# Performance work log

Measured on AMD Instinct MI355X. Metric: run time of the kernel, lower is better.

## Reference

```python
import jax, jax.numpy as jnp
import numpy as np
import math

BS = 32; N_NODE = 400; N = BS * N_NODE; E = 204800
D = 200; HS = 1024; SEQ = 512
N_NTYPE = 4; N_ETYPE = 38
HEADS = 4; DPH = D // HEADS
K_LAYERS = 5
EP1 = 1.0


def _lin(key, fi, fo, lead=None):
    shape = (fi, fo) if lead is None else (lead, fi, fo)
    return jax.random.normal(key, shape, jnp.float32) * 0.05


def setup_inputs() -> dict:
    key = jax.random.key(0)
    ks = jax.random.split(key, 20)
    inp = {}
    inp['hidden_states'] = jax.random.normal(ks[0], (BS, SEQ, HS), jnp.float32)
    inp['X'] = jax.random.normal(ks[1], (N, D), jnp.float32)
    inp['node_feature_extra'] = jax.random.normal(ks[2], (N, D), jnp.float32)
    inp['edge_index'] = jax.random.randint(ks[3], (2, E), 0, N)
    inp['edge_type'] = jax.random.randint(ks[4], (E,), 0, N_ETYPE)
    inp['node_type'] = jax.random.randint(ks[5], (N,), 0, N_NTYPE)
    inp['epoch'] = 0
    edge_in = N_ETYPE + 1 + 2 * N_NTYPE  # one-hot edge type (+self-loop) + head/tail node-type one-hots
    inp['We1'] = _lin(ks[6], edge_in, D); inp['be1'] = jnp.zeros((D,), jnp.float32)
    inp['We2'] = _lin(ks[7], D, D);       inp['be2'] = jnp.zeros((D,), jnp.float32)
    inp['Wkey'] = _lin(ks[8], 3 * D, D, K_LAYERS);  inp['bkey'] = jnp.zeros((K_LAYERS, D), jnp.float32)
    inp['Wmsg'] = _lin(ks[9], 3 * D, D, K_LAYERS);  inp['bmsg'] = jnp.zeros((K_LAYERS, D), jnp.float32)
    inp['Wqry'] = _lin(ks[10], 2 * D, D, K_LAYERS); inp['bqry'] = jnp.zeros((K_LAYERS, D), jnp.float32)
    inp['Wm1'] = _lin(ks[11], D, D, K_LAYERS);      inp['bm1'] = jnp.zeros((K_LAYERS, D), jnp.float32)
    inp['Wm2'] = _lin(ks[12], D, D, K_LAYERS);      inp['bm2'] = jnp.zeros((K_LAYERS, D), jnp.float32)
    inp['Wq_att'] = _lin(ks[13], D, D); inp['bq_att'] = jnp.zeros((D,), jnp.float32)
    inp['Wk_att'] = _lin(ks[14], D, D); inp['bk_att'] = jnp.zeros((D,), jnp.float32)
    inp['Wv_att'] = _lin(ks[15], D, D); inp['bv_att'] = jnp.zeros((D,), jnp.float32)
    inp['Wproj'] = _lin(ks[16], HS, D); inp['bproj'] = jnp.zeros((D,), jnp.float32)
    return inp


def _segment_softmax(scores, seg, n):
    m = jax.ops.segment_max(scores, seg, num_segments=n)
    m = jnp.where(jnp.isfinite(m), m, 0.0)
    e = jnp.exp(scores - m[seg])
    s = jax.ops.segment_sum(e, seg, num_segments=n)
    return e / (s[seg] + 1e-16)


def _gat_layer(X, nfe, src, dst, edge_emb, Wk, bk, Wm, bm, Wq, bq, W1, b1, W2, b2):
    n = X.shape[0]
    x = jnp.concatenate([X, nfe], axis=1)            # [N, 2D]
    x_i = x[dst]; x_j = x[src]                       # [E', 2D]
    key = (jnp.concatenate([x_i, edge_emb], 1) @ Wk + bk).reshape(-1, HEADS, DPH)
    msg = (jnp.concatenate([x_j, edge_emb], 1) @ Wm + bm).reshape(-1, HEADS, DPH)
    qry = ((x_i @ Wq + bq).reshape(-1, HEADS, DPH)) / math.sqrt(DPH)
    scores = (qry * key).sum(-1)                     # [E', HEADS]
    alpha = _segment_softmax(scores, src, n)
    cnt = jax.ops.segment_sum(jnp.ones_like(alpha[:, 0]), src, num_segments=n)[src]
    alpha = alpha * cnt[:, None]                     # scale by src out-degree (QAGNN GATConvE)
    out_msg = (msg * alpha[..., None]).reshape(-1, D)
    aggr = jax.ops.segment_sum(out_msg, dst, num_segments=n)
    out = jax.nn.relu(aggr @ W1 + b1) @ W2 + b2      # MLP, BatchNorm(eval) ~ identity
    sensitivity = jnp.max(jnp.linalg.norm(out, axis=-1))
    return out, sensitivity


def _forward(hidden_states, X, node_feature_extra, edge_index, edge_type, node_type,
             We1, be1, We2, be2, Wkey, bkey, Wmsg, bmsg, Wqry, bqry, Wm1, bm1, Wm2, bm2,
             Wq_att, bq_att, Wk_att, bk_att, Wv_att, bv_att, Wproj, bproj):
    n = X.shape[0]
    # self loops with edge type n_etype, as in GATConvE
    loop = jnp.arange(n)
    src = jnp.concatenate([edge_index[0], loop])
    dst = jnp.concatenate([edge_index[1], loop])
    et = jnp.concatenate([edge_type, jnp.full((n,), N_ETYPE, edge_type.dtype)])
    edge_vec = jax.nn.one_hot(et, N_ETYPE + 1, dtype=X.dtype)
    hvec = jax.nn.one_hot(node_type[src], N_NTYPE, dtype=X.dtype)
    tvec = jax.nn.one_hot(node_type[dst], N_NTYPE, dtype=X.dtype)
    # shared edge encoder (same edges each layer -> hoisted, identical math)
    edge_emb = jax.nn.relu(jnp.concatenate([edge_vec, hvec, tvec], 1) @ We1 + be1) @ We2 + be2
    context = hidden_states[:, 0, :] @ Wproj + bproj  # [bs, D]
    K = (context @ Wk_att + bk_att)[:, None, :]       # [bs, 1, D]
    V = (context @ Wv_att + bv_att)[:, None, :]
    nkey = jax.random.key(123)
    _X = X
    for li in range(K_LAYERS):
        _X, sens = _gat_layer(_X, node_feature_extra, src, dst, edge_emb,
                              Wkey[li], bkey[li], Wmsg[li], bmsg[li], Wqry[li], bqry[li],
                              Wm1[li], bm1[li], Wm2[li], bm2[li])
        _X = jax.nn.gelu(_X, approximate=False)
        Xb = _X.reshape(BS, N_NODE, D)
        Q = Xb @ Wq_att + bq_att
        Q = Q / jnp.maximum(jnp.linalg.norm(Q, axis=-1, keepdims=True), 1e-12)
        att = jnp.einsum('bnd,bmd->bnm', Q, K) / math.sqrt(D)  # [bs, n_node, 1]
        scale = jax.lax.stop_gradient(sens / (EP1 / 4.0))      # Laplace DP noise (non-diff in orig)
        noise = scale * jax.random.laplace(jax.random.fold_in(nkey, li), att.shape, att.dtype)
        att = att + noise
        _X = jnp.einsum('bnm,bmd->bnd', att, V).reshape(-1, D)
    return _X


def reference(hidden_states, X, node_feature_extra, edge_index, edge_type, node_type, epoch,
              We1, be1, We2, be2, Wkey, bkey, Wmsg, bmsg, Wqry, bqry, Wm1, bm1, Wm2, bm2,
              Wq_att, bq_att, Wk_att, bk_att, Wv_att, bv_att, Wproj, bproj):
    return _forward(hidden_states, X, node_feature_extra, edge_index, edge_type, node_type,
                    We1, be1, We2, be2, Wkey, bkey, Wmsg, bmsg, Wqry, bqry, Wm1, bm1, Wm2, bm2,
                    Wq_att, bq_att, Wk_att, bk_att, Wv_att, bv_att, Wproj, bproj)
```

## Files before the change

kernel.cpp:

```cpp
#include <hip/hip_runtime.h>
#include <stdint.h>

#define NBATCH 32
#define NNODE  400
#define NN     12800
#define NE     204800
#define EPE    217600
#define DD     200
#define NETYPE 38
#define NCOMBO 624
#define HSZ    1024
#define SEQQ   512
#define NL     5

__device__ __forceinline__ unsigned short f2bf(float x){
  uint32_t u = __float_as_uint(x);
  uint32_t r = (u + 0x7fffu + ((u>>16)&1u)) >> 16;
  return (unsigned short)r;
}

__device__ __forceinline__ uint32_t rotl32(uint32_t x, uint32_t d){ return (x<<d)|(x>>(32u-d)); }

__device__ void tf2x32(uint32_t k0, uint32_t k1, uint32_t x0, uint32_t x1,
                       uint32_t* o0, uint32_t* o1){
  uint32_t ks0=k0, ks1=k1, ks2=k0^k1^0x1BD11BDAu;
  uint32_t ks[3]={ks0,ks1,ks2};
  x0 += ks0; x1 += ks1;
  const uint32_t rotA[4]={13,15,26,6};
  const uint32_t rotB[4]={17,29,16,24};
  #pragma unroll
  for (int i=0;i<5;i++){
    const uint32_t* r = (i&1)? rotB : rotA;
    #pragma unroll
    for (int j=0;j<4;j++){ x0 += x1; x1 = rotl32(x1, r[j]); x1 ^= x0; }
    x0 += ks[(i+1)%3];
    x1 += ks[(i+2)%3] + (uint32_t)(i+1);
  }
  *o0=x0; *o1=x1;
}

__global__ void k_noise(float* noise){
  int i = blockIdx.x*256+threadIdx.x;
  if (i >= NL*NN) return;
  int l = i / NN, j = i % NN;
  uint32_t k0,k1,o0,o1,bits;
  tf2x32(0u,123u,0u,(uint32_t)l,&k0,&k1);
  tf2x32(k0,k1,0u,(uint32_t)j,&o0,&o1);
  bits = o0 ^ o1;
  uint32_t fb = (bits>>9) | 0x3f800000u;
  float f = __uint_as_float(fb) - 1.0f;
  const float minv = -0.99999994039535522461f;
  float u = fmaxf(minv, f*2.0f + minv);
  float s = (u>0.f)?1.f:((u<0.f)?-1.f:0.f);
  noise[i] = s*log1pf(-fabsf(u));
}

__global__ void k_edges(const int* eidx, int* outdeg, int* indeg){
  int e = blockIdx.x*256+threadIdx.x; if (e>=EPE) return;
  int s,dv;
  if (e < NE){ s = eidx[e]; dv = eidx[NE+e]; } else { s = dv = e-NE; }
  atomicAdd(&outdeg[s],1); atomicAdd(&indeg[dv],1);
}

__global__ void k_scan(const int* outdeg, const int* indeg, int* sstart, int* dstart){
  __shared__ int buf[2][1024];
  for (int which=0; which<2; ++which){
    const int* a = which? indeg : outdeg;
    int* o = which? dstart : sstart;
    int t = threadIdx.x;
    int c0 = t*13;
    int s = 0;
    for (int i=c0;i<c0+13;i++) if (i<NN) s += a[i];
    __syncthreads();
    buf[0][t]=s; __syncthreads();
    int cur=0;
    #pragma unroll
    for (int off=1; off<1024; off<<=1){
      int v = buf[cur][t];
      if (t>=off) v += buf[cur][t-off];
      buf[cur^1][t]=v; cur^=1; __syncthreads();
    }
    int run = buf[cur][t] - s;
    for (int i=c0;i<c0+13;i++) if (i<NN){ o[i]=run; run+=a[i]; }
    if (t==0) o[NN]=EPE;
  }
}

__global__ void k_scatter(const int* eidx, const int* etype, const int* ntype,
                          const int* sstart, const int* dstart, int* sfill, int* dfill,
                          int* s_dst, int* s_combo, int* d_src, int* d_combo, int* d_spos){
  int e = blockIdx.x*256+threadIdx.x; if (e>=EPE) return;
  int s,dv,et;
  if (e<NE){ s=eidx[e]; dv=eidx[NE+e]; et=etype[e]; } else { s=dv=e-NE; et=NETYPE; }
  int c = et*16 + ntype[s]*4 + ntype[dv];
  int p = sstart[s] + atomicAdd(&sfill[s],1);
  s_dst[p]=dv; s_combo[p]=c;
  int q = dstart[dv] + atomicAdd(&dfill[dv],1);
  d_src[q]=s; d_combo[q]=c; d_spos[q]=p;
}

__global__ void k_ehid(const float* We1, const float* be1, float* ehid){
  int i = blockIdx.x*256+threadIdx.x; if (i>=NCOMBO*DD) return;
  int c = i/DD, d = i%DD;
  int et=c>>4, ht=(c>>2)&3, tt=c&3;
  float v = We1[et*DD+d] + We1[(39+ht)*DD+d] + We1[(43+tt)*DD+d] + be1[d];
  ehid[i] = fmaxf(v,0.f);
}

__global__ void k_cvt_xcat(const float* X, const float* nfe, unsigned short* xbf){
  int i=blockIdx.x*256+threadIdx.x; if (i>=NN*448) return;
  int n=i/448, d=i%448;
  float v = (d<200)? X[(size_t)n*200+d] : (d<400)? nfe[(size_t)n*200+(d-200)] : 0.f;
  xbf[i] = f2bf(v);
}
__global__ void k_cvt_nfe(const float* nfe, unsigned short* nbf){
  int i=blockIdx.x*256+threadIdx.x; if (i>=NN*224) return;
  int n=i/224, d=i%224;
  nbf[i] = (d<200)? f2bf(nfe[(size_t)n*200+d]) : 0;
}

struct WJob { const float* src; unsigned short* dst; int Ksrc; int Kpad; };
struct WArgs { WJob j[26]; };
__global__ void k_wswz(WArgs a){
  WJob jb = a.j[blockIdx.z];
  int i = blockIdx.x*256+threadIdx.x;
  if (i >= jb.Kpad*256) return;
  int k = i>>8, n = i&255;
  unsigned short v = 0;
  if (k<jb.Ksrc && n<200) v = f2bf(jb.src[(size_t)k*200+n]);
  jb.dst[(((size_t)(k>>3))*256 + n)*8 + (k&7)] = v;
}

typedef __attribute__((ext_vector_type(8))) short bf16x8;
typedef __attribute__((ext_vector_type(4))) float f32x4;

struct MJob { const unsigned short* A; const unsigned short* B; const float* bias;
              float* C; unsigned short* Cbf; const float* r1v; const float* r1m;
              int relu; float scale; int gelu; };
struct MArgs { int Kpad; MJob j[3]; };

__global__ __launch_bounds__(256) void k_mgemm(MArgs g){
  const MJob jb = g.j[blockIdx.z];
  const int lane = threadIdx.x&63, w = threadIdx.x>>6;
  const int lr = lane&15, lk = lane>>4;
  const int m0 = blockIdx.y*128 + w*32;
  const int n0 = blockIdx.x*64;
  const int Kp = g.Kpad;
  f32x4 acc[2][4] = {};
  const unsigned short* a0 = jb.A + (size_t)(m0+lr)*Kp + lk*8;
  const unsigned short* a1 = a0 + (size_t)16*Kp;
  for (int ks=0; ks<Kp; ks+=32){
    bf16x8 af0 = *(const bf16x8*)(a0 + ks);
    bf16x8 af1 = *(const bf16x8*)(a1 + ks);
    const unsigned short* bb = jb.B + (((size_t)(ks>>3) + lk)*256 + n0 + lr)*8;
    bf16x8 b0 = *(const bf16x8*)(bb);
    bf16x8 b1 = *(const bf16x8*)(bb + 128);
    bf16x8 b2 = *(const bf16x8*)(bb + 256);
    bf16x8 b3 = *(const bf16x8*)(bb + 384);
    acc[0][0]=__builtin_amdgcn_mfma_f32_16x16x32_bf16(af0,b0,acc[0][0],0,0,0);
    acc[0][1]=__builtin_amdgcn_mfma_f32_16x16x32_bf16(af0,b1,acc[0][1],0,0,0);
    acc[0][2]=__builtin_amdgcn_mfma_f32_16x16x32_bf16(af0,b2,acc[0][2],0,0,0);
    acc[0][3]=__builtin_amdgcn_mfma_f32_16x16x32_bf16(af0,b3,acc[0][3],0,0,0);
    acc[1][0]=__builtin_amdgcn_mfma_f32_16x16x32_bf16(af1,b0,acc[1][0],0,0,0);
    acc[1][1]=__builtin_amdgcn_mfma_f32_16x16x32_bf16(af1,b1,acc[1][1],0,0,0);
    acc[1][2]=__builtin_amdgcn_mfma_f32_16x16x32_bf16(af1,b2,acc[1][2],0,0,0);
    acc[1][3]=__builtin_amdgcn_mfma_f32_16x16x32_bf16(af1,b3,acc[1][3],0,0,0);
  }
  #pragma unroll
  for (int mt=0; mt<2; ++mt){
    int mbase = m0 + mt*16 + lk*4;
    #pragma unroll
    for (int nt=0; nt<4; ++nt){
      int n = n0 + nt*16 + lr;
      #pragma unroll
      for (int r=0;r<4;r++){
        int m = mbase + r;
        float v = acc[mt][nt][r];
        if (n < 200){
          if (jb.r1v)  v += jb.r1v[m]*jb.r1m[(size_t)(m/NNODE)*200 + n];
          if (jb.bias) v += jb.bias[n];
          v *= jb.scale;
          if (jb.relu) v = fmaxf(v, 0.f);
          if (jb.C)    jb.C[(size_t)m*200 + n] = v;
          if (jb.Cbf){
            float o = jb.gelu? 0.5f*v*(1.0f+erff(v*0.70710678118654752440f)) : v;
            jb.Cbf[(size_t)m*224 + n] = f2bf(o);
          }
        } else if (jb.Cbf && n < 224){
          jb.Cbf[(size_t)m*224 + n] = 0;
        }
      }
    }
  }
}

struct RJob { const float* A; const float* W; const float* bias; float* C; int K; size_t lda; };
struct RArgs { RJob j[12]; float* part; int NS; int Kc; };
__global__ __launch_bounds__(256) void k_rowpart(RArgs a){
  RJob jb = a.j[blockIdx.z];
  int m = blockIdx.x, s = blockIdx.y;
  int k0 = s*a.Kc, k1 = k0 + a.Kc; if (k1 > jb.K) k1 = jb.K;
  int kc = k1 - k0;
  __shared__ float row[128];
  const float* ap = jb.A + (size_t)m*jb.lda + k0;
  for (int k=threadIdx.x; k<kc; k+=256) row[k]=ap[k];
  __syncthreads();
  int n = threadIdx.x;
  if (n < 200){
    float acc = 0.f;
    const float* wp = jb.W + (size_t)k0*200 + n;
    for (int kk=0; kk<kc; ++kk) acc += row[kk]*wp[(size_t)kk*200];
    a.part[(((size_t)blockIdx.z*32 + m)*8 + s)*200 + n] = acc;
  }
}
__global__ __launch_bounds__(256) void k_rowred(RArgs a){
  RJob jb = a.j[blockIdx.z];
  int m = blockIdx.x, n = threadIdx.x;
  if (n >= 200) return;
  float acc = jb.bias? jb.bias[n] : 0.f;
  for (int s=0; s<a.NS; ++s) acc += a.part[(((size_t)blockIdx.z*32 + m)*8 + s)*200 + n];
  jb.C[(size_t)m*200+n] = acc;
}

struct Job {
  const float* A; const float* W; const float* bias; float* C;
  const float* r1v; const float* r1m; int relu;
};
struct GArgs { int M,N,K,lda; Job j[12]; };

#define BMT 64
#define BNT 64
#define BKT 16

__global__ __launch_bounds__(256) void k_gemm(GArgs g){
  const Job jb = g.j[blockIdx.z];
  const int m0 = blockIdx.y*BMT, n0 = blockIdx.x*BNT;
  __shared__ float As[BKT][BMT+4];
  __shared__ float Bs[BKT][BNT+4];
  float acc[4][4]={};
  const int t = threadIdx.x;
  const int tx = t & 15, ty = t >> 4;
  for (int k0=0; k0<g.K; k0+=BKT){
    {
      int r = t>>2, cq = t&3;
      int m = m0+r, k = k0+cq*4;
      float4 v = make_float4(0.f,0.f,0.f,0.f);
      if (m < g.M && k < g.K){
        if (k+3 < g.K) v = *(const float4*)(jb.A + (size_t)m*g.lda + k);
        else {
          const float* ap = jb.A + (size_t)m*g.lda;
          float tm[4]={0.f,0.f,0.f,0.f};
          for (int qq=0;qq<4;qq++) if (k+qq<g.K) tm[qq]=ap[k+qq];
          v = make_float4(tm[0],tm[1],tm[2],tm[3]);
        }
      }
      As[cq*4+0][r]=v.x; As[cq*4+1][r]=v.y; As[cq*4+2][r]=v.z; As[cq*4+3][r]=v.w;
    }
    {
      int r = t>>4, cq = t&15;
      int k = k0+r, n = n0+cq*4;
      float4 v = make_float4(0.f,0.f,0.f,0.f);
      if (k < g.K && n < g.N){
        if (n+3 < g.N) v = *(const float4*)(jb.W + (size_t)k*g.N + n);
        else { const float* wp = jb.W + (size_t)k*g.N;
          float tm[4]={0.f,0.f,0.f,0.f};
          for (int qq=0;qq<4;qq++) if (n+qq<g.N) tm[qq]=wp[n+qq];
          v = make_float4(tm[0],tm[1],tm[2],tm[3]); }
      }
      Bs[r][cq*4+0]=v.x; Bs[r][cq*4+1]=v.y; Bs[r][cq*4+2]=v.z; Bs[r][cq*4+3]=v.w;
    }
    __syncthreads();
    int kend = g.K-k0; if (kend>BKT) kend=BKT;
    for (int kk=0;kk<kend;kk++){
      float4 av = *(const float4*)&As[kk][ty*4];
      float4 bv = *(const float4*)&Bs[kk][tx*4];
      float a[4]={av.x,av.y,av.z,av.w};
      float b[4]={bv.x,bv.y,bv.z,bv.w};
      #pragma unroll
      for (int i=0;i<4;i++){
        #pragma unroll
        for (int jq=0;jq<4;jq++) acc[i][jq] += a[i]*b[jq];
      }
    }
    __syncthreads();
  }
  #pragma unroll
  for (int i=0;i<4;i++){
    int m = m0+ty*4+i; if (m>=g.M) continue;
    int bidx = m / NNODE;
    #pragma unroll
    for (int jq=0;jq<4;jq++){
      int n = n0+tx*4+jq; if (n>=g.N) continue;
      float v = acc[i][jq];
      if (jb.bias) v += jb.bias[n];
      if (jb.r1v)  v += jb.r1v[m]*jb.r1m[(size_t)bidx*g.N + n];
      if (jb.relu) v = fmaxf(v,0.f);
      jb.C[(size_t)m*g.N+n] = v;
    }
  }
}

__global__ void k_prep(const float* qv, const float* Ak, float* ps){
  int wid = threadIdx.x>>6, lane = threadIdx.x&63;
  int n = blockIdx.x*4 + wid; if (n>=NN) return;
  float acch[4]={0.f,0.f,0.f,0.f};
  for (int d=lane; d<DD; d+=64)
    acch[d/50] += qv[(size_t)n*DD+d]*Ak[(size_t)n*DD+d];
  for (int off=1; off<64; off<<=1){
    #pragma unroll
    for (int h=0;h<4;h++) acch[h] += __shfl_xor(acch[h], off);
  }
  if (lane==0){
    #pragma unroll
    for (int h=0;h<4;h++) ps[n*4+h]=acch[h];
  }
}

__global__ __launch_bounds__(256) void k_score(const int* s_dst, const int* s_combo, const float* qv,
                        const float* Bk, const float* ps, float* scores){
  int p = blockIdx.x*64 + (threadIdx.x>>2);
  if (p>=EPE) return;
  int sub = threadIdx.x&3;
  int dv = s_dst[p], c = s_combo[p];
  const float4* qr = (const float4*)(qv + (size_t)dv*DD);
  const float4* br = (const float4*)(Bk + (size_t)c*DD);
  float acc[4]={0.f,0.f,0.f,0.f};
  #pragma unroll
  for (int i=0;i<13;i++){
    int q = sub + 4*i;
    if (q < 50){
      float4 a = qr[q], b = br[q];
      int d = q*4;
      acc[(d+0)/50] += a.x*b.x;
      acc[(d+1)/50] += a.y*b.y;
      acc[(d+2)/50] += a.z*b.z;
      acc[(d+3)/50] += a.w*b.w;
    }
  }
  #pragma unroll
  for (int off=1; off<4; off<<=1){
    #pragma unroll
    for (int h=0;h<4;h++) acc[h] += __shfl_xor(acc[h], off);
  }
  scores[(size_t)p*4+sub] = ps[dv*4+sub] + acc[sub];
}

__global__ void k_softmax(const int* sstart, float* scores){
  int n = blockIdx.x;
  int st = sstart[n], en = sstart[n+1];
  int cnt = en-st;
  int t = threadIdx.x;
  float mx = -3.402823466e38f;
  for (int i=t; i<cnt*4; i+=64) mx = fmaxf(mx, scores[(size_t)(st+(i>>2))*4 + (i&3)]);
  for (int off=4; off<64; off<<=1) mx = fmaxf(mx, __shfl_xor(mx,off));
  float sm=0.f;
  for (int i=t; i<cnt*4; i+=64) sm += expf(scores[(size_t)(st+(i>>2))*4 + (i&3)] - mx);
  for (int off=4; off<64; off<<=1) sm += __shfl_xor(sm,off);
  float scale = (float)cnt / (sm + 1e-16f);
  for (int i=t; i<cnt*4; i+=64){
    size_t idx=(size_t)(st+(i>>2))*4+(i&3);
    scores[idx] = expf(scores[idx]-mx)*scale;
  }
}

__global__ void k_aggr(const int* dstart, const int* d_src, const int* d_combo, const int* d_spos,
                       const float* alpha, const float* Am, const float* Bm,
                       unsigned short* aggr_bf){
  int v = blockIdx.x; int d = threadIdx.x; if (d>=224) return;
  if (d>=200){ aggr_bf[(size_t)v*224+d]=0; return; }
  int h = d/50;
  int st=dstart[v], en=dstart[v+1];
  float acc=0.f;
  for (int q=st;q<en;q++){
    int s=d_src[q], c=d_combo[q], p=d_spos[q];
    float a = alpha[(size_t)p*4+h];
    acc += a*(Am[(size_t)s*DD+d] + Bm[(size_t)c*DD+d]);
  }
  aggr_bf[(size_t)v*224+d]=f2bf(acc);
}

__global__ void k_sens(const float* out, float* sens2, int l){
  __shared__ float smax[4];
  int wid = threadIdx.x>>6, lane = threadIdx.x&63;
  int gw = blockIdx.x*4 + wid;
  float mx = 0.f;
  for (int n = gw; n < NN; n += 256){
    const float4* row = (const float4*)(out + (size_t)n*DD);
    float ss = 0.f;
    if (lane < 50){ float4 v = row[lane]; ss = v.x*v.x + v.y*v.y + v.z*v.z + v.w*v.w; }
    for (int off=1; off<64; off<<=1) ss += __shfl_xor(ss, off);
    mx = fmaxf(mx, ss);
  }
  if (lane==0) smax[wid] = mx;
  __syncthreads();
  if (threadIdx.x==0){
    float m = fmaxf(fmaxf(smax[0],smax[1]),fmaxf(smax[2],smax[3]));
    atomicMax((int*)&sens2[l], __float_as_int(m));
  }
}

__global__ void k_att(const float* Q, const float* Katt, const float* Vatt,
                      const float* sens2, const float* noise, int l,
                      float* att, float* outX){
  int wid=threadIdx.x>>6, lane=threadIdx.x&63;
  int n=blockIdx.x*4+wid; if (n>=NN) return;
  int b=n/NNODE;
  float qq=0.f, qk=0.f;
  for (int d=lane; d<DD; d+=64){
    float q=Q[(size_t)n*DD+d];
    qq += q*q; qk += q*Katt[b*DD+d];
  }
  for (int off=1;off<64;off<<=1){ qq+=__shfl_xor(qq,off); qk+=__shfl_xor(qk,off); }
  float nrm = fmaxf(sqrtf(qq), 1e-12f);
  float a = (qk/nrm) * 0.07071067811865475244f;
  a += 4.0f*sqrtf(sens2[l]) * noise[(size_t)l*NN + n];
  if (lane==0) att[n]=a;
  if (outX){
    for (int d=lane; d<DD; d+=64) outX[(size_t)n*DD+d] = a*Vatt[b*DD+d];
  }
}

static inline Job mkjob(const float* A, const float* W, const float* bias, float* C,
                        const float* r1v, const float* r1m, int relu){
  Job j; j.A=A; j.W=W; j.bias=bias; j.C=C; j.r1v=r1v; j.r1m=r1m; j.relu=relu; return j;
}

static inline void gemm_launch(hipStream_t stream, int M,int N,int K,int lda,
                               const Job* jobs, int nj){
  GArgs g; g.M=M; g.N=N; g.K=K; g.lda=lda;
  for (int i=0;i<nj;i++) g.j[i]=jobs[i];
  for (int i=nj;i<12;i++) g.j[i]=jobs[0];
  dim3 grid((N+BNT-1)/BNT,(M+BMT-1)/BMT,nj);
  k_gemm<<<grid,256,0,stream>>>(g);
}

static inline RJob mkrjob(const float* A, const float* W, const float* bias, float* C,
                          int K, size_t lda){
  RJob j; j.A=A; j.W=W; j.bias=bias; j.C=C; j.K=K; j.lda=lda; return j;
}

static inline void rgemm_launch(hipStream_t stream, const RJob* jobs, int nj,
                                float* part, int NS, int Kc){
  RArgs a;
  for (int i=0;i<nj;i++) a.j[i]=jobs[i];
  for (int i=nj;i<12;i++) a.j[i]=jobs[0];
  a.part = part; a.NS = NS; a.Kc = Kc;
  k_rowpart<<<dim3(NBATCH,NS,nj),256,0,stream>>>(a);
  k_rowred <<<dim3(NBATCH,1,nj),256,0,stream>>>(a);
}

static inline MJob mkmjob(const unsigned short* A, const unsigned short* B, const float* bias,
                          float* C, unsigned short* Cbf, const float* r1v, const float* r1m,
                          int relu, float scale, int gelu){
  MJob j; j.A=A; j.B=B; j.bias=bias; j.C=C; j.Cbf=Cbf; j.r1v=r1v; j.r1m=r1m;
  j.relu=relu; j.scale=scale; j.gelu=gelu; return j;
}

static inline void mgemm_launch(hipStream_t stream, int Kpad, const MJob* jobs, int nj){
  MArgs a; a.Kpad=Kpad;
  for (int i=0;i<nj;i++) a.j[i]=jobs[i];
  for (int i=nj;i<3;i++) a.j[i]=jobs[0];
  k_mgemm<<<dim3(4,100,nj),256,0,stream>>>(a);
}

extern "C" void kernel_launch(void* const* d_in, const int* in_sizes, int n_in,
                              void* d_out, int out_size, void* d_ws, size_t ws_size,
                              hipStream_t stream){
  const float* hs    = (const float*)d_in[0];
  const float* X     = (const float*)d_in[1];
  const float* nfe   = (const float*)d_in[2];
  const int*   eidx  = (const int*)d_in[3];
  const int*   etype = (const int*)d_in[4];
  const int*   ntype = (const int*)d_in[5];
  const float* We1   = (const float*)d_in[7];
  const float* be1   = (const float*)d_in[8];
  const float* We2   = (const float*)d_in[9];
  const float* be2   = (const float*)d_in[10];
  const float* Wkey  = (const float*)d_in[11];
  const float* bkey  = (const float*)d_in[12];
  const float* Wmsg  = (const float*)d_in[13];
  const float* bmsg  = (const float*)d_in[14];
  const float* Wqry  = (const float*)d_in[15];
  const float* bqry  = (const float*)d_in[16];
  const float* Wm1   = (const float*)d_in[17];
  const float* bm1   = (const float*)d_in[18];
  const float* Wm2   = (const float*)d_in[19];
  const float* bm2   = (const float*)d_in[20];
  const float* Wq_att= (const float*)d_in[21];
  const float* bq_att= (const float*)d_in[22];
  const float* Wk_att= (const float*)d_in[23];
  const float* bk_att= (const float*)d_in[24];
  const float* Wv_att= (const float*)d_in[25];
  const float* bv_att= (const float*)d_in[26];
  const float* Wproj = (const float*)d_in[27];
  const float* bproj = (const float*)d_in[28];
  float* outp = (float*)d_out;

  char* cur = (char*)d_ws;
  auto allocf = [&](size_t n)->float*{ float* p=(float*)cur; cur += ((n*4+255)/256)*256; return p; };
  auto alloci = [&](size_t n)->int*  { int*   p=(int*)cur;   cur += ((n*4+255)/256)*256; return p; };
  auto allocb = [&](size_t n)->unsigned short*{ unsigned short* p=(unsigned short*)cur; cur += ((n*2+255)/256)*256; return p; };

  float* noise  = allocf((size_t)NL*NN);
  float* ehid   = allocf((size_t)NCOMBO*DD);
  float* eemb   = allocf((size_t)NCOMBO*DD);
  float* Bk     = allocf((size_t)NL*NCOMBO*DD);
  float* Bm     = allocf((size_t)NL*NCOMBO*DD);
  float* context= allocf((size_t)NBATCH*DD);
  float* Katt   = allocf((size_t)NBATCH*DD);
  float* Vatt   = allocf((size_t)NBATCH*DD);
  float* CKk    = allocf((size_t)4*NBATCH*DD);
  float* CKm    = allocf((size_t)4*NBATCH*DD);
  float* CKq    = allocf((size_t)4*NBATCH*DD);
  float* Ak     = allocf((size_t)NN*DD);
  float* Am     = allocf((size_t)NN*DD);
  float* Aq     = allocf((size_t)NN*DD);
  float* ps     = allocf((size_t)NN*4);
  float* scores = allocf((size_t)EPE*4);
  float* Q      = allocf((size_t)NN*DD);
  float* outb   = allocf((size_t)NN*DD);
  float* att    = allocf((size_t)NN);
  float* sens2  = allocf(8);
  float* rpart  = allocf((size_t)12*NBATCH*8*200);
  unsigned short* xcat_bf = allocb((size_t)NN*448);
  unsigned short* nfe_bf  = allocb((size_t)NN*224);
  unsigned short* aggr_bf = allocb((size_t)NN*224);
  unsigned short* tmp1_bf = allocb((size_t)NN*224);
  unsigned short* gelu_bf = allocb((size_t)NN*224);
  unsigned short* wkx0  = allocb((size_t)448*256);
  unsigned short* wmx0  = allocb((size_t)448*256);
  unsigned short* wqx0  = allocb((size_t)448*256);
  unsigned short* wkN   = allocb((size_t)4*224*256);
  unsigned short* wmN   = allocb((size_t)4*224*256);
  unsigned short* wqN   = allocb((size_t)4*224*256);
  unsigned short* wm1s  = allocb((size_t)5*224*256);
  unsigned short* wm2s  = allocb((size_t)5*224*256);
  unsigned short* wqatts= allocb((size_t)224*256);
  int* sstart = alloci(NN+1);
  int* dstart = alloci(NN+1);
  int* outdeg = alloci(NN);
  int* indeg  = alloci(NN);
  int* sfill  = alloci(NN);
  int* dfill  = alloci(NN);
  int* s_dst  = alloci(EPE);
  int* s_combo= alloci(EPE);
  int* d_src  = alloci(EPE);
  int* d_combo= alloci(EPE);
  int* d_spos = alloci(EPE);
  if ((size_t)(cur-(char*)d_ws) > ws_size) return;

  hipMemsetAsync(outdeg,0,(size_t)4*NN*4,stream);
  hipMemsetAsync(sens2 ,0,32,stream);

  k_noise<<<(NL*NN+255)/256,256,0,stream>>>(noise);
  k_edges<<<(EPE+255)/256,256,0,stream>>>(eidx,outdeg,indeg);
  k_scan<<<1,1024,0,stream>>>(outdeg,indeg,sstart,dstart);
  k_scatter<<<(EPE+255)/256,256,0,stream>>>(eidx,etype,ntype,sstart,dstart,sfill,dfill,
                                            s_dst,s_combo,d_src,d_combo,d_spos);
  k_ehid<<<(NCOMBO*DD+255)/256,256,0,stream>>>(We1,be1,ehid);
  { Job j = mkjob(ehid,We2,be2,eemb,0,0,0); gemm_launch(stream,NCOMBO,DD,DD,DD,&j,1); }
  { Job js[10];
    for (int l=0;l<NL;l++){
      js[2*l+0]=mkjob(eemb, Wkey + (size_t)l*600*DD + 400*DD, 0, Bk + (size_t)l*NCOMBO*DD, 0,0,0);
      js[2*l+1]=mkjob(eemb, Wmsg + (size_t)l*600*DD + 400*DD, bmsg + (size_t)l*DD,
                      Bm + (size_t)l*NCOMBO*DD, 0,0,0);
    }
    gemm_launch(stream,NCOMBO,DD,DD,DD,js,10);
  }
  k_cvt_xcat<<<(NN*448+255)/256,256,0,stream>>>(X,nfe,xcat_bf);
  k_cvt_nfe<<<(NN*224+255)/256,256,0,stream>>>(nfe,nfe_bf);
  { WArgs wa; int wn=0;
    auto addw=[&](const float* s, unsigned short* d, int Ks, int Kp){
      wa.j[wn].src=s; wa.j[wn].dst=d; wa.j[wn].Ksrc=Ks; wa.j[wn].Kpad=Kp; wn++; };
    addw(Wkey, wkx0, 400,448);
    addw(Wmsg, wmx0, 400,448);
    addw(Wqry, wqx0, 400,448);
    for (int l=1;l<NL;l++){
      addw(Wkey + (size_t)l*600*DD + 200*DD, wkN + (size_t)(l-1)*224*256, 200,224);
      addw(Wmsg + (size_t)l*600*DD + 200*DD, wmN + (size_t)(l-1)*224*256, 200,224);
      addw(Wqry + (size_t)l*400*DD + 200*DD, wqN + (size_t)(l-1)*224*256, 200,224);
    }
    for (int l=0;l<NL;l++){
      addw(Wm1 + (size_t)l*DD*DD, wm1s + (size_t)l*224*256, 200,224);
      addw(Wm2 + (size_t)l*DD*DD, wm2s + (size_t)l*224*256, 200,224);
    }
    addw(Wq_att, wqatts, 200,224);
    k_wswz<<<dim3(448,1,wn),256,0,stream>>>(wa);
  }
  { RJob j = mkrjob(hs, Wproj, bproj, context, HSZ, (size_t)SEQQ*HSZ);
    rgemm_launch(stream, &j, 1, rpart, 8, 128); }
  { RJob js[2] = { mkrjob(context, Wk_att, bk_att, Katt, DD, DD),
                   mkrjob(context, Wv_att, bv_att, Vatt, DD, DD) };
    rgemm_launch(stream, js, 2, rpart, 2, 100); }
  { RJob js[12];
    for (int l=1;l<NL;l++){
      js[3*(l-1)+0]=mkrjob(Vatt, Wkey + (size_t)l*600*DD, 0, CKk + (size_t)(l-1)*NBATCH*DD, DD, DD);
      js[3*(l-1)+1]=mkrjob(Vatt, Wmsg + (size_t)l*600*DD, 0, CKm + (size_t)(l-1)*NBATCH*DD, DD, DD);
      js[3*(l-1)+2]=mkrjob(Vatt, Wqry + (size_t)l*400*DD, 0, CKq + (size_t)(l-1)*NBATCH*DD, DD, DD);
    }
    rgemm_launch(stream, js, 12, rpart, 4, 50);
  }

  const float invs = 0.14142135623730950488f;
  for (int l=0;l<NL;l++){
    const float* bkey_l = bkey + (size_t)l*DD;
    const float* bqry_l = bqry + (size_t)l*DD;
    const float* Bk_l = Bk + (size_t)l*NCOMBO*DD;
    const float* Bm_l = Bm + (size_t)l*NCOMBO*DD;

    if (l==0){
      MJob js[3] = { mkmjob(xcat_bf, wkx0, bkey_l, Ak, 0, 0,0,0, 1.f,0),
                     mkmjob(xcat_bf, wmx0, 0,      Am, 0, 0,0,0, 1.f,0),
                     mkmjob(xcat_bf, wqx0, bqry_l, Aq, 0, 0,0,0, invs,0) };
      mgemm_launch(stream,448,js,3);
    } else {
      const float* ckk = CKk + (size_t)(l-1)*NBATCH*DD;
      const float* ckm = CKm + (size_t)(l-1)*NBATCH*DD;
      const float* ckq = CKq + (size_t)(l-1)*NBATCH*DD;
      MJob js[3] = { mkmjob(nfe_bf, wkN + (size_t)(l-1)*224*256, bkey_l, Ak, 0, att, ckk, 0, 1.f,0),
                     mkmjob(nfe_bf, wmN + (size_t)(l-1)*224*256, 0,      Am, 0, att, ckm, 0, 1.f,0),
                     mkmjob(nfe_bf, wqN + (size_t)(l-1)*224*256, bqry_l, Aq, 0, att, ckq, 0, invs,0) };
      mgemm_launch(stream,224,js,3);
    }
    k_prep<<<NN/4,256,0,stream>>>(Aq,Ak,ps);
    k_score<<<(EPE*4+255)/256,256,0,stream>>>(s_dst,s_combo,Aq,Bk_l,ps,scores);
    k_softmax<<<NN,64,0,stream>>>(sstart,scores);
    k_aggr<<<NN,256,0,stream>>>(dstart,d_src,d_combo,d_spos,scores,Am,Bm_l,aggr_bf);
    { MJob j = mkmjob(aggr_bf, wm1s + (size_t)l*224*256, bm1 + (size_t)l*DD, 0, tmp1_bf, 0,0,1, 1.f,0);
      mgemm_launch(stream,224,&j,1); }
    { MJob j = mkmjob(tmp1_bf, wm2s + (size_t)l*224*256, bm2 + (size_t)l*DD, outb, gelu_bf, 0,0,0, 1.f,1);
      mgemm_launch(stream,224,&j,1); }
    k_sens<<<64,256,0,stream>>>(outb,sens2,l);
    { MJob j = mkmjob(gelu_bf, wqatts, bq_att, Q, 0, 0,0,0, 1.f,0);
      mgemm_launch(stream,224,&j,1); }
    k_att<<<NN/4,256,0,stream>>>(Q,Katt,Vatt,sens2,noise,l,att,(l==NL-1)? outp : (float*)0);
  }
}
```

Measured before the change: 1.248 ms.

## Store message tensors in bf16 and vectorize edge aggregation across waves

The message-projection GEMM now writes its output Am directly as bf16 with row stride 200, and Bm is converted once to bf16. The aggregation kernel is rewritten so each wave processes every fourth incoming edge, with 25 lanes each loading 8 bf16 values and a float4 of attention weights, followed by a shared-memory reduction across the four waves. This halves gather bytes and widens loads in the edge-gather loop, at the cost of extra bf16 rounding in the messages and an added conversion kernel.

```diff
diff --git a/kernel.cpp b/kernel.cpp
--- a/kernel.cpp
+++ b/kernel.cpp
@@ -17,6 +17,9 @@
   uint32_t u = __float_as_uint(x);
   uint32_t r = (u + 0x7fffu + ((u>>16)&1u)) >> 16;
   return (unsigned short)r;
+}
+__device__ __forceinline__ float bf2f(unsigned short b){
+  return __uint_as_float(((uint32_t)b)<<16);
 }
 
 __device__ __forceinline__ uint32_t rotl32(uint32_t x, uint32_t d){ return (x<<d)|(x>>(32u-d)); }
@@ -118,6 +121,10 @@
   int n=i/224, d=i%224;
   nbf[i] = (d<200)? f2bf(nfe[(size_t)n*200+d]) : 0;
 }
+__global__ void k_cvt_flat(const float* src, unsigned short* dst, int n){
+  int i=blockIdx.x*256+threadIdx.x; if (i>=n) return;
+  dst[i] = f2bf(src[i]);
+}
 
 struct WJob { const float* src; unsigned short* dst; int Ksrc; int Kpad; };
 struct WArgs { WJob j[26]; };
@@ -136,7 +143,7 @@
 
 struct MJob { const unsigned short* A; const unsigned short* B; const float* bias;
               float* C; unsigned short* Cbf; const float* r1v; const float* r1m;
-              int relu; float scale; int gelu; };
+              int relu; float scale; int gelu; int cbfs; };
 struct MArgs { int Kpad; MJob j[3]; };
 
 __global__ __launch_bounds__(256) void k_mgemm(MArgs g){
@@ -184,9 +191,9 @@
           if (jb.C)    jb.C[(size_t)m*200 + n] = v;
           if (jb.Cbf){
             float o = jb.gelu? 0.5f*v*(1.0f+erff(v*0.70710678118654752440f)) : v;
-            jb.Cbf[(size_t)m*224 + n] = f2bf(o);
+            jb.Cbf[(size_t)m*jb.cbfs + n] = f2bf(o);
           }
-        } else if (jb.Cbf && n < 224){
+        } else if (jb.Cbf && jb.cbfs==224 && n < 224){
           jb.Cbf[(size_t)m*224 + n] = 0;
         }
       }
@@ -363,20 +370,42 @@
   }
 }
 
-__global__ void k_aggr(const int* dstart, const int* d_src, const int* d_combo, const int* d_spos,
-                       const float* alpha, const float* Am, const float* Bm,
+__global__ __launch_bounds__(256) void k_aggr(const int* dstart, const int* d_src, const int* d_combo,
+                       const int* d_spos, const float* alpha,
+                       const unsigned short* Am, const unsigned short* Bm,
                        unsigned short* aggr_bf){
-  int v = blockIdx.x; int d = threadIdx.x; if (d>=224) return;
-  if (d>=200){ aggr_bf[(size_t)v*224+d]=0; return; }
-  int h = d/50;
+  __shared__ float red[4][200];
+  int v = blockIdx.x;
+  int w = threadIdx.x>>6, lane = threadIdx.x&63;
   int st=dstart[v], en=dstart[v+1];
-  float acc=0.f;
-  for (int q=st;q<en;q++){
-    int s=d_src[q], c=d_combo[q], p=d_spos[q];
-    float a = alpha[(size_t)p*4+h];
-    acc += a*(Am[(size_t)s*DD+d] + Bm[(size_t)c*DD+d]);
-  }
-  aggr_bf[(size_t)v*224+d]=f2bf(acc);
+  float acc[8]={0.f,0.f,0.f,0.f,0.f,0.f,0.f,0.f};
+  if (lane < 25){
+    int h[8];
+    #pragma unroll
+    for (int j=0;j<8;j++) h[j] = (lane*8+j)/50;
+    for (int q=st+w; q<en; q+=4){
+      int s=d_src[q], c=d_combo[q], p=d_spos[q];
+      float4 al4 = *(const float4*)(alpha + (size_t)p*4);
+      bf16x8 am = *(const bf16x8*)(Am + (size_t)s*200 + lane*8);
+      bf16x8 bm = *(const bf16x8*)(Bm + (size_t)c*200 + lane*8);
+      const float* alp = &al4.x;
+      #pragma unroll
+      for (int j=0;j<8;j++){
+        float a = alp[h[j]];
+        acc[j] += a*(bf2f((unsigned short)am[j]) + bf2f((unsigned short)bm[j]));
+      }
+    }
+    #pragma unroll
+    for (int j=0;j<8;j++) red[w][lane*8+j]=acc[j];
+  }
+  __syncthreads();
+  int d = threadIdx.x;
+  if (d < 200){
+    float r = red[0][d]+red[1][d]+red[2][d]+red[3][d];
+    aggr_bf[(size_t)v*224+d]=f2bf(r);
+  } else if (d < 224){
+    aggr_bf[(size_t)v*224+d]=0;
+  }
 }
 
 __global__ void k_sens(const float* out, float* sens2, int l){
@@ -451,9 +480,9 @@
 
 static inline MJob mkmjob(const unsigned short* A, const unsigned short* B, const float* bias,
                           float* C, unsigned short* Cbf, const float* r1v, const float* r1m,
-                          int relu, float scale, int gelu){
+                          int relu, float scale, int gelu, int cbfs){
   MJob j; j.A=A; j.B=B; j.bias=bias; j.C=C; j.Cbf=Cbf; j.r1v=r1v; j.r1m=r1m;
-  j.relu=relu; j.scale=scale; j.gelu=gelu; return j;
+  j.relu=relu; j.scale=scale; j.gelu=gelu; j.cbfs=cbfs; return j;
 }
 
 static inline void mgemm_launch(hipStream_t stream, int Kpad, const MJob* jobs, int nj){
@@ -513,7 +542,6 @@
   float* CKm    = allocf((size_t)4*NBATCH*DD);
   float* CKq    = allocf((size_t)4*NBATCH*DD);
   float* Ak     = allocf((size_t)NN*DD);
-  float* Am     = allocf((size_t)NN*DD);
   float* Aq     = allocf((size_t)NN*DD);
   float* ps     = allocf((size_t)NN*4);
   float* scores = allocf((size_t)EPE*4);
@@ -522,6 +550,8 @@
   float* att    = allocf((size_t)NN);
   float* sens2  = allocf(8);
   float* rpart  = allocf((size_t)12*NBATCH*8*200);
+  unsigned short* am_bf   = allocb((size_t)NN*200);
+  unsigned short* bm_bf   = allocb((size_t)NL*NCOMBO*DD);
   unsigned short* xcat_bf = allocb((size_t)NN*448);
   unsigned short* nfe_bf  = allocb((size_t)NN*224);
   unsigned short* aggr_bf = allocb((size_t)NN*224);
@@ -567,6 +597,7 @@
     }
     gemm_launch(stream,NCOMBO,DD,DD,DD,js,10);
   }
+  k_cvt_flat<<<(NL*NCOMBO*DD+255)/256,256,0,stream>>>(Bm, bm_bf, NL*NCOMBO*DD);
   k_cvt_xcat<<<(NN*448+255)/256,256,0,stream>>>(X,nfe,xcat_bf);
   k_cvt_nfe<<<(NN*224+255)/256,256,0,stream>>>(nfe,nfe_bf);
   { WArgs wa; int wn=0;
@@ -606,32 +637,32 @@
     const float* bkey_l = bkey + (size_t)l*DD;
     const float* bqry_l = bqry + (size_t)l*DD;
     const float* Bk_l = Bk + (size_t)l*NCOMBO*DD;
-    const float* Bm_l = Bm + (size_t)l*NCOMBO*DD;
+    const unsigned short* Bm_l = bm_bf + (size_t)l*NCOMBO*DD;
 
     if (l==0){
-      MJob js[3] = { mkmjob(xcat_bf, wkx0, bkey_l, Ak, 0, 0,0,0, 1.f,0),
-                     mkmjob(xcat_bf, wmx0, 0,      Am, 0, 0,0,0, 1.f,0),
-                     mkmjob(xcat_bf, wqx0, bqry_l, Aq, 0, 0,0,0, invs,0) };
+      MJob js[3] = { mkmjob(xcat_bf, wkx0, bkey_l, Ak, 0,     0,0,0, 1.f,0, 224),
+                     mkmjob(xcat_bf, wmx0, 0,      0,  am_bf, 0,0,0, 1.f,0, 200),
+                     mkmjob(xcat_bf, wqx0, bqry_l, Aq, 0,     0,0,0, invs,0, 224) };
       mgemm_launch(stream,448,js,3);
     } else {
       const float* ckk = CKk + (size_t)(l-1)*NBATCH*DD;
       const float* ckm = CKm + (size_t)(l-1)*NBATCH*DD;
       const float* ckq = CKq + (size_t)(l-1)*NBATCH*DD;
-      MJob js[3] = { mkmjob(nfe_bf, wkN + (size_t)(l-1)*224*256, bkey_l, Ak, 0, att, ckk, 0, 1.f,0),
-                     mkmjob(nfe_bf, wmN + (size_t)(l-1)*224*256, 0,      Am, 0, att, ckm, 0, 1.f,0),
-                     mkmjob(nfe_bf, wqN + (size_t)(l-1)*224*256, bqry_l, Aq, 0, att, ckq, 0, invs,0) };
+      MJob js[3] = { mkmjob(nfe_bf, wkN + (size_t)(l-1)*224*256, bkey_l, Ak, 0,     att, ckk, 0, 1.f,0, 224),
+                     mkmjob(nfe_bf, wmN + (size_t)(l-1)*224*256, 0,      0,  am_bf, att, ckm, 0, 1.f,0, 200),
+                     mkmjob(nfe_bf, wqN + (size_t)(l-1)*224*256, bqry_l, Aq, 0,     att, ckq, 0, invs,0, 224) };
       mgemm_launch(stream,224,js,3);
     }
     k_prep<<<NN/4,256,0,stream>>>(Aq,Ak,ps);
     k_score<<<(EPE*4+255)/256,256,0,stream>>>(s_dst,s_combo,Aq,Bk_l,ps,scores);
     k_softmax<<<NN,64,0,stream>>>(sstart,scores);
-    k_aggr<<<NN,256,0,stream>>>(dstart,d_src,d_combo,d_spos,scores,Am,Bm_l,aggr_bf);
-    { MJob j = mkmjob(aggr_bf, wm1s + (size_t)l*224*256, bm1 + (size_t)l*DD, 0, tmp1_bf, 0,0,1, 1.f,0);
+    k_aggr<<<NN,256,0,stream>>>(dstart,d_src,d_combo,d_spos,scores,am_bf,Bm_l,aggr_bf);
+    { MJob j = mkmjob(aggr_bf, wm1s + (size_t)l*224*256, bm1 + (size_t)l*DD, 0, tmp1_bf, 0,0,1, 1.f,0, 224);
       mgemm_launch(stream,224,&j,1); }
-    { MJob j = mkmjob(tmp1_bf, wm2s + (size_t)l*224*256, bm2 + (size_t)l*DD, outb, gelu_bf, 0,0,0, 1.f,1);
+    { MJob j = mkmjob(tmp1_bf, wm2s + (size_t)l*224*256, bm2 + (size_t)l*DD, outb, gelu_bf, 0,0,0, 1.f,1, 224);
       mgemm_launch(stream,224,&j,1); }
     k_sens<<<64,256,0,stream>>>(outb,sens2,l);
-    { MJob j = mkmjob(gelu_bf, wqatts, bq_att, Q, 0, 0,0,0, 1.f,0);
+    { MJob j = mkmjob(gelu_bf, wqatts, bq_att, Q, 0, 0,0,0, 1.f,0, 224);
       mgemm_launch(stream,224,&j,1); }
     k_att<<<NN/4,256,0,stream>>>(Q,Katt,Vatt,sens2,noise,l,att,(l==NL-1)? outp : (float*)0);
   }
```

New measurement: 1.269 ms. About the same (+1.7%).
